# Kernel optimization log

Hardware: AMD Instinct MI355X
Metric: run time of the kernel (lower is better)

## Reference

```python
import jax, jax.numpy as jnp
import numpy as np
from jax import lax

# pywt 'db6' rec_lo (scaling filter). dec_lo = rec_lo[::-1]; pytorch_wavelets
# stores dec filters flipped for conv (=correlation), so analysis correlation
# filters are exactly rec_lo and rec_hi = qmf(rec_lo). Synthesis filters for
# conv_transpose are rec_lo/rec_hi unflipped -> same arrays.
_DB6 = np.array([0.11154074335008017, 0.4946238903983854, 0.7511339080215775,
                 0.3152503517092432, -0.22626469396516913, -0.12976686756709563,
                 0.09750160558707936, 0.02752286553001629, -0.031582039318031156,
                 0.0005538422009938016, 0.004777257511010651, -0.00107730108499558],
                dtype=np.float32)
_QMF = (_DB6[::-1].copy() * ((-1.0) ** np.arange(12))).astype(np.float32)
H0, H1 = jnp.asarray(_DB6), jnp.asarray(_QMF)
LF, J = 12, 3
BATCH, SEQ_LEN, CH = 128, 720, 321
COMP_L = [99, 365, 188, 99]   # [yl, yh1, yh2, yh3] for seq_len=720
OUT_L = [22, 57, 34, 22]      # same decomposition of red_len=104


def afb1d(x):
    """One-level analysis filter bank, mode='symmetric'. x: [B,C,N]."""
    B, C, N = x.shape
    out = (N + LF - 1) // 2                      # pywt dwt_coeff_len (symmetric)
    p = 2 * (out - 1) - N + LF
    xp = jnp.pad(x, ((0, 0), (0, 0), (p // 2, (p + 1) // 2)), mode='symmetric')
    w = jnp.stack([H0, H1])[:, None, :]          # [2,1,LF]
    y = lax.conv_general_dilated(xp.reshape(B * C, 1, -1), w, (2,), 'VALID',
                                 dimension_numbers=('NCH', 'OIH', 'NCH'))
    y = y.reshape(B, C, 2, out)
    return y[:, :, 0], y[:, :, 1]


def sfb1d(lo, hi):
    """One-level synthesis bank == conv_transpose1d(stride=2, padding=LF-2)."""
    B, C, Lin = lo.shape
    z = jnp.stack([lo, hi], axis=2).reshape(B * C, 2, Lin)
    w = jnp.stack([H0[::-1], H1[::-1]])[None]    # [1,2,LF], flipped for corr
    y = lax.conv_general_dilated(z, w, (1,), ((1, 1),), lhs_dilation=(2,),
                                 dimension_numbers=('NCH', 'OIH', 'NCH'))
    return y.reshape(B, C, -1)                   # length 2*Lin + 2 - LF


def sinusoidal_pe(n_pos, d):
    pos = jnp.arange(n_pos, dtype=jnp.float32)[:, None]
    div = jnp.exp(jnp.arange(0, d, 2, dtype=jnp.float32) * (-np.log(10000.0) / d))
    pe = jnp.zeros((n_pos, d), jnp.float32)
    pe = pe.at[:, 0::2].set(jnp.sin(pos * div))
    pe = pe.at[:, 1::2].set(jnp.cos(pos * div[: d // 2]))
    return pe


def _forward(x, qws, qbs, kws, kbs, pws, pbs, iws, als, bes):
    mean = lax.stop_gradient(jnp.mean(x, axis=1, keepdims=True))
    std = lax.stop_gradient(jnp.sqrt(jnp.var(x, axis=1, keepdims=True) + 1e-5))
    xc = jnp.transpose((x - mean) / std, (0, 2, 1))      # [B,C,L]
    yl, yh = xc, []
    for _ in range(J):
        yl, hi = afb1d(yl)
        yh.append(hi)
    decomps = [yl] + yh                                  # lengths COMP_L
    preds = []
    for i, comp in enumerate(decomps):
        B, C, L = comp.shape
        Q = jnp.tanh(comp @ qws[i].T + qbs[i])           # [B,C,L]
        K = jnp.tanh(comp @ kws[i].T + kbs[i])
        scores = jnp.einsum('bcl,bcs->bls', Q, K) / (L ** 0.5)
        weighted = jnp.mean(jnp.tanh(scores), axis=1)    # [B,S] (equal per channel)
        cum = jnp.flip(jnp.cumsum(jnp.flip(weighted, -1), -1), -1)
        P = jax.nn.softmax(cum * als[i][0], axis=-1)
        idxs = jnp.arange(L, dtype=jnp.float32)
        win = jnp.sum(P * idxs, axis=-1)[:, None, None]  # soft truncation [B,1,1]
        mask = jax.nn.sigmoid((idxs[None, None, :] - win) * bes[i][0])
        pred = (comp * mask) @ pws[i].T + pbs[i]         # [B,C,O]
        pred = jax.nn.softmax(iws[i], axis=1) * (pred + sinusoidal_pe(C, pred.shape[-1])[None])
        preds.append(pred)
    ll = preds[0]
    for h in preds[:0:-1]:                               # coarsest high band first
        if ll.shape[-1] > h.shape[-1]:
            ll = ll[..., : h.shape[-1]]
        ll = sfb1d(ll, h)
    return ll, mean, std


def setup_inputs() -> dict:
    key = jax.random.key(0)
    ks = jax.random.split(key, 64)
    inp = {'x': jax.random.normal(ks[0], (BATCH, SEQ_LEN, CH), jnp.float32)}
    k = 1
    for i, (L, O) in enumerate(zip(COMP_L, OUT_L)):
        s = 1.0 / np.sqrt(L)                             # torch Linear default init
        inp[f'qw{i}'] = jax.random.uniform(ks[k], (L, L), jnp.float32, -s, s); k += 1
        inp[f'qb{i}'] = jax.random.uniform(ks[k], (L,), jnp.float32, -s, s); k += 1
        inp[f'kw{i}'] = jax.random.uniform(ks[k], (L, L), jnp.float32, -s, s); k += 1
        inp[f'kb{i}'] = jax.random.uniform(ks[k], (L,), jnp.float32, -s, s); k += 1
        inp[f'pw{i}'] = jnp.full((O, L), 1.0 / L, jnp.float32)
        inp[f'pb{i}'] = jnp.zeros((O,), jnp.float32)
        inp[f'iw{i}'] = jnp.ones((1, CH, O), jnp.float32)
        inp[f'al{i}'] = jnp.full((1,), 10.0, jnp.float32)
        inp[f'be{i}'] = jnp.full((1,), 10.0, jnp.float32)
    return inp


def reference(x, qw0, qb0, kw0, kb0, pw0, pb0, iw0, al0, be0,
              qw1, qb1, kw1, kb1, pw1, pb1, iw1, al1, be1,
              qw2, qb2, kw2, kb2, pw2, pb2, iw2, al2, be2,
              qw3, qb3, kw3, kb3, pw3, pb3, iw3, al3, be3):
    return _forward(x, [qw0, qw1, qw2, qw3], [qb0, qb1, qb2, qb3],
                    [kw0, kw1, kw2, kw3], [kb0, kb1, kb2, kb3],
                    [pw0, pw1, pw2, pw3], [pb0, pb1, pb2, pb3],
                    [iw0, iw1, iw2, iw3], [al0, al1, al2, al3],
                    [be0, be1, be2, be3])
```

## Files before the change

kernel.cpp:

```cpp
#include <hip/hip_runtime.h>
#include <hip/hip_bf16.h>
#include <math.h>

namespace {
constexpr int kB  = 128;
constexpr int kC  = 321;
constexpr int kN0 = 720;
constexpr int kCp = 384;
}

typedef __attribute__((ext_vector_type(8))) short short8;
typedef __attribute__((ext_vector_type(4))) float floatx4;

__constant__ float c_h0[12] = {
  0.11154074335008017f, 0.4946238903983854f, 0.7511339080215775f,
  0.3152503517092432f, -0.22626469396516913f, -0.12976686756709563f,
  0.09750160558707936f, 0.02752286553001629f, -0.031582039318031156f,
  0.0005538422009938016f, 0.004777257511010651f, -0.00107730108499558f};
__constant__ float c_h1[12] = {
  -0.00107730108499558f, -0.004777257511010651f, 0.0005538422009938016f,
  0.031582039318031156f, 0.02752286553001629f, -0.09750160558707936f,
  -0.12976686756709563f, 0.22626469396516913f, 0.3152503517092432f,
  -0.7511339080215775f, 0.4946238903983854f, -0.11154074335008017f};
__constant__ float c_h0r[12] = {
  -0.00107730108499558f, 0.004777257511010651f, 0.0005538422009938016f,
  -0.031582039318031156f, 0.02752286553001629f, 0.09750160558707936f,
  -0.12976686756709563f, -0.22626469396516913f, 0.3152503517092432f,
  0.7511339080215775f, 0.4946238903983854f, 0.11154074335008017f};
__constant__ float c_h1r[12] = {
  -0.11154074335008017f, 0.4946238903983854f, -0.7511339080215775f,
  0.3152503517092432f, 0.22626469396516913f, -0.12976686756709563f,
  -0.09750160558707936f, 0.02752286553001629f, 0.031582039318031156f,
  0.0005538422009938016f, -0.004777257511010651f, -0.00107730108499558f};

__device__ __forceinline__ float fast_tanh(float x) {
  float e = __expf(2.f * x);
  return 1.f - 2.f / (e + 1.f);
}
__device__ __forceinline__ unsigned short f2b(float f) {
  __hip_bfloat16 h = __float2bfloat16(f);
  return __builtin_bit_cast(unsigned short, h);
}

__device__ __forceinline__ void gload16(const unsigned short* g, short* l) {
  __builtin_amdgcn_global_load_lds(
      (const __attribute__((address_space(1))) unsigned int*)g,
      (__attribute__((address_space(3))) unsigned int*)l, 16, 0, 0);
}

__global__ void __launch_bounds__(128) partial_ms_kernel(
    const float* __restrict__ x, float* __restrict__ ps, float* __restrict__ ps2) {
  int b = blockIdx.x, chunk = blockIdx.y;
  int c = blockIdx.z * 128 + threadIdx.x;
  if (c >= kC) return;
  const float* xb = x + (size_t)b * kN0 * kC + c;
  int t0 = chunk * 90;
  float s = 0.f, s2 = 0.f;
#pragma unroll 15
  for (int i = 0; i < 90; ++i) {
    float v = xb[(size_t)(t0 + i) * kC];
    s += v; s2 += v * v;
  }
  ps [(b * 8 + chunk) * kC + c] = s;
  ps2[(b * 8 + chunk) * kC + c] = s2;
}

__global__ void __launch_bounds__(256) finalize_ms_kernel(
    const float* __restrict__ ps, const float* __restrict__ ps2,
    float* __restrict__ mout, float* __restrict__ sout,
    float* __restrict__ meanw, float* __restrict__ invw) {
  int i = blockIdx.x * 256 + threadIdx.x;
  if (i >= kB * kC) return;
  int b = i / kC, c = i - b * kC;
  float s = 0.f, s2 = 0.f;
#pragma unroll
  for (int k = 0; k < 8; ++k) { s += ps[(b * 8 + k) * kC + c]; s2 += ps2[(b * 8 + k) * kC + c]; }
  float mean = s * (1.f / (float)kN0);
  float var = s2 * (1.f / (float)kN0) - mean * mean;
  float sd = sqrtf(var + 1e-5f);
  mout[i] = mean; sout[i] = sd;
  meanw[i] = mean; invw[i] = 1.f / sd;
}

__device__ __forceinline__ int sym_reflect(int t, int N) {
  t = (t < 0) ? (-1 - t) : t;
  t = (t >= N) ? (2 * N - 1 - t) : t;
  return t;
}

template <bool NORM, bool LO_F32, bool LO_BF16>
__global__ void __launch_bounds__(256) dwt_fused_kernel(
    const float* __restrict__ in, const float* __restrict__ meanw,
    const float* __restrict__ invw, float* __restrict__ loF,
    unsigned short* __restrict__ loB, unsigned short* __restrict__ hiB,
    int N, int L, int Lp) {
  __shared__ float xs[138][64];
  __shared__ unsigned short los[64][72];
  __shared__ unsigned short his[64][72];
  const int b = blockIdx.z;
  const int n0 = blockIdx.x * 64, c0 = blockIdx.y * 64;
  const int tid = threadIdx.x;
  const int cl = tid & 63, wv = tid >> 6;
  const int c = c0 + cl;
  const int t0 = 2 * n0 - 10;
  const float* ib = in + (size_t)b * N * kC;
  float mean = 0.f, inv = 1.f;
  if (NORM && c < kC) { mean = meanw[b * kC + c]; inv = invw[b * kC + c]; }
  for (int r = wv; r < 138; r += 4) {
    int t = sym_reflect(t0 + r, N);
    float v = (c < kC) ? ib[(size_t)t * kC + c] : 0.f;
    if (NORM) v = (v - mean) * inv;
    xs[r][cl] = v;
  }
  __syncthreads();
#pragma unroll 4
  for (int k = 0; k < 16; ++k) {
    int nl = wv + 4 * k;
    int n = n0 + nl;
    float a0 = 0.f, a1 = 0.f;
    int base = 2 * nl;
#pragma unroll
    for (int j = 0; j < 12; ++j) {
      float v = xs[base + j][cl];
      a0 += v * c_h0[j]; a1 += v * c_h1[j];
    }
    bool valid = (n < L) && (c < kC);
    if (LO_F32 && valid) loF[((size_t)b * L + n) * kC + c] = a0;
    if (LO_BF16) los[cl][nl] = f2b(valid ? a0 : 0.f);
    his[cl][nl] = f2b(valid ? a1 : 0.f);
  }
  __syncthreads();
  int row = tid >> 2, part = tid & 3;
  size_t dst = ((size_t)b * kCp + c0 + row) * Lp + n0 + part * 16;
  *(uint4*)(hiB + dst)     = *(const uint4*)&his[row][part * 16];
  *(uint4*)(hiB + dst + 8) = *(const uint4*)&his[row][part * 16 + 8];
  if (LO_BF16) {
    *(uint4*)(loB + dst)     = *(const uint4*)&los[row][part * 16];
    *(uint4*)(loB + dst + 8) = *(const uint4*)&los[row][part * 16 + 8];
  }
}

struct WcArgs { const float* src[8]; unsigned short* dst[8]; int L[8]; int Lp[8]; };
__global__ void __launch_bounds__(256) wconv_all_kernel(WcArgs a) {
  int lvl = blockIdx.y;
  int Lp = a.Lp[lvl], L = a.L[lvl];
  int i = blockIdx.x * 256 + threadIdx.x;
  if (i >= Lp * Lp) return;
  int p = i / Lp, l = i - p * Lp;
  a.dst[lvl][i] = f2b((p < L && l < L) ? a.src[lvl][(size_t)p * L + l] : 0.f);
}

template <int NT>
__device__ __forceinline__ void qk_kloop(
    short* smem, const unsigned short* s0, const unsigned short* s1,
    const unsigned short* s2, bool extra, int lo0, int lo1, int lo2,
    int ar, int bb, floatx4 (&acc)[2][4]) {
  gload16(s0, &smem[lo0]);
  gload16(s1, &smem[lo1]);
  if (extra) gload16(s2, &smem[lo2]);
  __syncthreads();
#pragma unroll
  for (int kt = 0; kt < NT; ++kt) {
    if (kt + 1 < NT) {
      const int phn = ((kt + 1) & 1) * 10240;
      const int go = (kt + 1) * 32;
      gload16(s0 + go, &smem[phn + lo0]);
      gload16(s1 + go, &smem[phn + lo1]);
      if (extra) gload16(s2 + go, &smem[phn + lo2]);
    }
    const int ph = (kt & 1) * 10240;
    short8 aq = *(const short8*)&smem[ph + ar];
    short8 ak = *(const short8*)&smem[ph + 4096 + ar];
    short8 bv[4];
#pragma unroll
    for (int ni = 0; ni < 4; ++ni)
      bv[ni] = *(const short8*)&smem[ph + 8192 + bb + ni * 512];
#pragma unroll
    for (int ni = 0; ni < 4; ++ni) {
      acc[0][ni] = __builtin_amdgcn_mfma_f32_16x16x32_bf16(aq, bv[ni], acc[0][ni], 0, 0, 0);
      acc[1][ni] = __builtin_amdgcn_mfma_f32_16x16x32_bf16(ak, bv[ni], acc[1][ni], 0, 0, 0);
    }
    __syncthreads();
  }
}

struct QKAllArgs {
  const unsigned short* W[8];
  const unsigned short* Xt[4];
  const float* bias[8];
  unsigned short* Y[8];
  int Lp[4], L[4], yOff[4];
};
__global__ void __launch_bounds__(512, 8) qk_all_kernel(QKAllArgs a) {
  const int y = blockIdx.y;
  const int lvl = (y >= a.yOff[1]) + (y >= a.yOff[2]) + (y >= a.yOff[3]);
  const int Lp = a.Lp[lvl], L = a.L[lvl];
  const int pBase = (y - a.yOff[lvl]) * 128;
  const unsigned short* W0 = a.W[2 * lvl]     + (size_t)pBase * Lp;
  const unsigned short* W1 = a.W[2 * lvl + 1] + (size_t)pBase * Lp;
  const int b = blockIdx.z;
  const int cBase = blockIdx.x * 64;
  const int tid = threadIdx.x;
  const int ln = tid & 63;
  const int w = __builtin_amdgcn_readfirstlane(tid >> 6);
  __shared__ short smem[2 * 320 * 32];
  floatx4 acc[2][4] = {};
  const unsigned short* Xb = a.Xt[lvl] + ((size_t)b * kCp + cBase) * Lp;
  const int lr = ln >> 2;
  const int kOfs = ((((ln & 3) - ((ln >> 3) & 3)) & 3)) * 8;
  const bool extra = (w < 4);
  const int o0 = 2 * w, o1 = 2 * w + 1;
  const unsigned short* s0 = (extra ? (W0 + (size_t)(o0 * 16 + lr) * Lp)
                                    : (W1 + (size_t)((o0 - 8) * 16 + lr) * Lp)) + kOfs;
  const unsigned short* s1 = (extra ? (W0 + (size_t)(o1 * 16 + lr) * Lp)
                                    : (W1 + (size_t)((o1 - 8) * 16 + lr) * Lp)) + kOfs;
  const unsigned short* s2 = Xb + (size_t)(w * 16 + lr) * Lp + kOfs;
  const int lo0 = o0 * 512, lo1 = o1 * 512, lo2 = (16 + w) * 512;
  const int sc = ((((ln >> 4) + ((ln >> 1) & 3)) & 3)) * 8;
  const int ar = (w * 16 + (ln & 15)) * 32 + sc;
  const int bb = (ln & 15) * 32 + sc;
  const int nt = (L + 31) >> 5;
  if (nt == 4)      qk_kloop<4>(smem, s0, s1, s2, extra, lo0, lo1, lo2, ar, bb, acc);
  else if (nt == 6) qk_kloop<6>(smem, s0, s1, s2, extra, lo0, lo1, lo2, ar, bb, acc);
  else              qk_kloop<12>(smem, s0, s1, s2, extra, lo0, lo1, lo2, ar, bb, acc);
  short* yq = smem;
  short* yk = smem + 8192;
#pragma unroll
  for (int s = 0; s < 2; ++s) {
    const float* bias = a.bias[2 * lvl + s];
    short* dstL = s ? yk : yq;
#pragma unroll
    for (int r = 0; r < 4; ++r) {
      int pl = w * 16 + (ln >> 4) * 4 + r;
      int p = pBase + pl;
      bool pv = (p < L);
      float bvf = pv ? bias[p] : 0.f;
#pragma unroll
      for (int ni = 0; ni < 4; ++ni) {
        int cl = ni * 16 + (ln & 15);
        float v = fast_tanh(acc[s][ni][r] + bvf);
        if (s == 1 && cBase + cl >= kC) v = 0.f;
        dstL[pl * 64 + (cl ^ ((pl & 7) << 3))] = (short)f2b(v);
      }
    }
  }
  __syncthreads();
#pragma unroll
  for (int s = 0; s < 2; ++s) {
    unsigned short* Yd = a.Y[2 * lvl + s];
    const short* srcL = s ? yk : yq;
#pragma unroll
    for (int j = 0; j < 2; ++j) {
      int idx = tid * 2 + j;
      int row = idx >> 3;
      if (pBase + row >= L) continue;
      int ch = idx & 7;
      int pch = ch ^ (row & 7);
      uint4 vv = *(const uint4*)&srcL[row * 64 + pch * 8];
      *(uint4*)(Yd + ((size_t)b * Lp + pBase + row) * kCp + cBase + ch * 8) = vv;
    }
  }
}

struct ScAllArgs {
  const unsigned short* Q[4]; const unsigned short* K[4];
  float* wgt[4];
  int Lp[4], L[4], tOff[4];
  float scale[4];
};
__global__ void __launch_bounds__(512, 8) scores_all_kernel(ScAllArgs a) {
  const int bid = blockIdx.x;
  const int wg = (bid & 7) * 240 + (bid >> 3);
  const int t = wg % 15;
  const int b = wg / 15;
  const int lvl = (t >= a.tOff[1]) + (t >= a.tOff[2]) + (t >= a.tOff[3]);
  const int rel = t - a.tOff[lvl];
  const int Lp = a.Lp[lvl], L = a.L[lvl];
  const int pt = Lp >> 7;
  const int sBase = (rel % pt) * 128;
  const int lBase = (rel / pt) * 128;
  const int tid = threadIdx.x;
  const int ln = tid & 63;
  const int w = __builtin_amdgcn_readfirstlane(tid >> 6);
  const int wm = w & 3, wn = w >> 2;
  __shared__ short smem[2 * 256 * 32];
  __shared__ float red[128];
  floatx4 acc[2][4] = {};
  const unsigned short* Qp = a.Q[lvl] + ((size_t)b * Lp + lBase) * kCp;
  const unsigned short* Kp = a.K[lvl] + ((size_t)b * Lp + sBase) * kCp;
  const int lr = ln >> 2;
  const int kOfs = ((((ln & 3) - ((ln >> 3) & 3)) & 3)) * 8;
  const int o0 = 2 * w, o1 = 2 * w + 1;
  const unsigned short* s0 = ((o0 < 8) ? (Qp + (size_t)(o0 * 16 + lr) * kCp)
                                       : (Kp + (size_t)((o0 - 8) * 16 + lr) * kCp)) + kOfs;
  const unsigned short* s1 = ((o1 < 8) ? (Qp + (size_t)(o1 * 16 + lr) * kCp)
                                       : (Kp + (size_t)((o1 - 8) * 16 + lr) * kCp)) + kOfs;
  const int lo0 = o0 * 512, lo1 = o1 * 512;
  const int sc = ((((ln >> 4) + ((ln >> 1) & 3)) & 3)) * 8;
  const int aBase = (wm * 32 + (ln & 15)) * 32 + sc;
  const int bBase = 4096 + (wn * 64 + (ln & 15)) * 32 + sc;
  gload16(s0, &smem[lo0]);
  gload16(s1, &smem[lo1]);
  if (tid < 128) red[tid] = 0.f;
  __syncthreads();
  constexpr int NT = (kC + 31) >> 5;
#pragma unroll
  for (int kt = 0; kt < NT; ++kt) {
    if (kt + 1 < NT) {
      const int phn = ((kt + 1) & 1) * 8192;
      const int go = (kt + 1) * 32;
      gload16(s0 + go, &smem[phn + lo0]);
      gload16(s1 + go, &smem[phn + lo1]);
    }
    const int ph = (kt & 1) * 8192;
    short8 av[2], bv[4];
#pragma unroll
    for (int mi = 0; mi < 2; ++mi)
      av[mi] = *(const short8*)&smem[ph + aBase + mi * 512];
#pragma unroll
    for (int ni = 0; ni < 4; ++ni)
      bv[ni] = *(const short8*)&smem[ph + bBase + ni * 512];
#pragma unroll
    for (int mi = 0; mi < 2; ++mi)
#pragma unroll
      for (int ni = 0; ni < 4; ++ni)
        acc[mi][ni] = __builtin_amdgcn_mfma_f32_16x16x32_bf16(av[mi], bv[ni], acc[mi][ni], 0, 0, 0);
    __syncthreads();
  }
  const float scale = a.scale[lvl];
#pragma unroll
  for (int ni = 0; ni < 4; ++ni) {
    float p = 0.f;
#pragma unroll
    for (int mi = 0; mi < 2; ++mi)
#pragma unroll
      for (int r = 0; r < 4; ++r) {
        int l = lBase + wm * 32 + mi * 16 + (ln >> 4) * 4 + r;
        if (l < L) p += fast_tanh(acc[mi][ni][r] * scale);
      }
    p += __shfl_xor(p, 16);
    p += __shfl_xor(p, 32);
    if ((ln & 48) == 0) atomicAdd(&red[wn * 64 + ni * 16 + (ln & 15)], p);
  }
  __syncthreads();
  if (tid < 128) {
    int s = sBase + tid;
    if (s < L) atomicAdd(&a.wgt[lvl][(size_t)b * L + s], red[tid]);
  }
}

struct WinIwArgs {
  const float* wgt[4]; const float* al[4]; const float* be[4];
  float* mask[4]; int L[4];
  const float* iw[4]; float* sm[4]; int O[4];
};
__global__ void __launch_bounds__(64) winiw_kernel(WinIwArgs a) {
  int bx = blockIdx.x;
  int lane = threadIdx.x;
  if (bx < 512) {
    int lvl = bx >> 7, b = bx & 127;
    int L = a.L[lvl];
    const float* wgt = a.wgt[lvl] + (size_t)b * L;
    float al = a.al[lvl][0], be = a.be[lvl][0];
    float invL = 1.f / (float)L;
    int chunk = (L + 63) >> 6;
    int s0 = lane * chunk;
    float v[6];
    float csum = 0.f;
    for (int i = chunk - 1; i >= 0; --i) {
      int s = s0 + i;
      float xv = (s < L) ? wgt[s] * invL : 0.f;
      csum += xv; v[i] = csum;
    }
    float tot = csum;
    for (int o = 1; o < 64; o <<= 1) {
      float t = __shfl_down(tot, o);
      if (lane + o < 64) tot += t;
    }
    float excl = tot - csum;
    float m = -1e30f;
    for (int i = 0; i < chunk; ++i)
      if (s0 + i < L) m = fmaxf(m, al * (v[i] + excl));
    for (int o = 32; o; o >>= 1) m = fmaxf(m, __shfl_xor(m, o));
    float sum = 0.f, num = 0.f;
    for (int i = 0; i < chunk; ++i) {
      int s = s0 + i;
      if (s < L) { float e = __expf(al * (v[i] + excl) - m); sum += e; num += e * (float)s; }
    }
    for (int o = 32; o; o >>= 1) { sum += __shfl_xor(sum, o); num += __shfl_xor(num, o); }
    float win = num / sum;
    float* mk = a.mask[lvl] + (size_t)b * L;
    for (int i = 0; i < chunk; ++i) {
      int s = s0 + i;
      if (s < L) mk[s] = 1.f / (1.f + __expf(-((float)s - win) * be));
    }
  } else {
    int x = bx - 512;
    int lvl, o;
    if (x < 22) { lvl = 0; o = x; }
    else if (x < 79) { lvl = 1; o = x - 22; }
    else if (x < 113) { lvl = 2; o = x - 79; }
    else { lvl = 3; o = x - 113; }
    int O = a.O[lvl];
    const float* iw = a.iw[lvl];
    float m = -1e30f;
    for (int c = lane; c < kC; c += 64) m = fmaxf(m, iw[c * O + o]);
    for (int k = 32; k; k >>= 1) m = fmaxf(m, __shfl_xor(m, k));
    float sum = 0.f;
    for (int c = lane; c < kC; c += 64) sum += __expf(iw[c * O + o] - m);
    for (int k = 32; k; k >>= 1) sum += __shfl_xor(sum, k);
    float inv = 1.f / sum;
    for (int c = lane; c < kC; c += 64) a.sm[lvl][c * O + o] = __expf(iw[c * O + o] - m) * inv;
  }
}

struct PredAllArgs {
  const unsigned short* Xt[4];
  const float* PW[4]; const float* PB[4]; const float* MK[4]; const float* SM[4];
  float* OUT[4];
  int L[4], Lp[4], O[4];
};
__global__ void __launch_bounds__(256) pred_all_kernel(PredAllArgs a) {
  const int lvl = blockIdx.y;
  const int L = a.L[lvl], Lp = a.Lp[lvl], O = a.O[lvl];
  const float* PW = a.PW[lvl];
  const int b = blockIdx.z;
  const int cBase = blockIdx.x * 128;
  const int tid = threadIdx.x;
  const int ln = tid & 63, w = tid >> 6;
  __shared__ short As[64 * 40];
  __shared__ short Bs[128 * 40];
  floatx4 acc[8] = {};
  const unsigned short* Xb = a.Xt[lvl] + ((size_t)b * kCp + cBase) * Lp;
  const float* mk = a.MK[lvl] + (size_t)b * L;
  for (int lc = 0; lc < Lp; lc += 32) {
    {
      int o = tid >> 2, j0 = (tid & 3) * 8;
      alignas(16) unsigned short tmp[8];
#pragma unroll
      for (int j = 0; j < 8; ++j) {
        int l = lc + j0 + j;
        float v = (o < O && l < L) ? PW[(size_t)o * L + l] * mk[l] : 0.f;
        tmp[j] = f2b(v);
      }
      *(uint4*)&As[o * 40 + j0] = *(const uint4*)tmp;
    }
#pragma unroll
    for (int q = 0; q < 2; ++q) {
      int ch = tid * 2 + q;
      int row = ch >> 2, pos = ch & 3;
      *(uint4*)(&Bs[row * 40 + pos * 8]) = *(const uint4*)(Xb + (size_t)row * Lp + lc + pos * 8);
    }
    __syncthreads();
    short8 av = *(const short8*)&As[(w * 16 + (ln & 15)) * 40 + (ln >> 4) * 8];
#pragma unroll
    for (int ni = 0; ni < 8; ++ni) {
      short8 bb = *(const short8*)&Bs[(ni * 16 + (ln & 15)) * 40 + (ln >> 4) * 8];
      acc[ni] = __builtin_amdgcn_mfma_f32_16x16x32_bf16(av, bb, acc[ni], 0, 0, 0);
    }
    __syncthreads();
  }
  const float negln = -logf(10000.f) / (float)O;
#pragma unroll
  for (int ni = 0; ni < 8; ++ni) {
    int c = cBase + ni * 16 + (ln & 15);
    if (c >= kC) continue;
#pragma unroll
    for (int r = 0; r < 4; ++r) {
      int o = w * 16 + (ln >> 4) * 4 + r;
      if (o >= O) continue;
      float dv = __expf(negln * (float)(2 * (o >> 1)));
      float ang = (float)c * dv;
      float pe = (o & 1) ? cosf(ang) : sinf(ang);
      a.OUT[lvl][((size_t)b * O + o) * kC + c] = a.SM[lvl][c * O + o] * (acc[ni][r] + a.PB[lvl][o] + pe);
    }
  }
}

__global__ void __launch_bounds__(256) sfb_fused_kernel(
    const float* __restrict__ P0, const float* __restrict__ P1,
    const float* __restrict__ P2, const float* __restrict__ P3,
    float* __restrict__ out) {
  __shared__ float p0s[22][32], p3s[22][32], p2s[34][32], p1s[57][32];
  __shared__ float r1s[34][32], r2s[58][32];
  __shared__ float outs[104][33];
  int b = blockIdx.y, c0 = blockIdx.x * 32;
  int tid = threadIdx.x;
  int cl = tid & 31, r = tid >> 5;
  int c = c0 + cl;
  bool cv = c < kC;
  for (int o = r; o < 22; o += 8) {
    p0s[o][cl] = cv ? P0[((size_t)b * 22 + o) * kC + c] : 0.f;
    p3s[o][cl] = cv ? P3[((size_t)b * 22 + o) * kC + c] : 0.f;
  }
  for (int o = r; o < 34; o += 8) p2s[o][cl] = cv ? P2[((size_t)b * 34 + o) * kC + c] : 0.f;
  for (int o = r; o < 57; o += 8) p1s[o][cl] = cv ? P1[((size_t)b * 57 + o) * kC + c] : 0.f;
  __syncthreads();
  for (int n = r; n < 34; n += 8) {
    float acc = 0.f;
#pragma unroll
    for (int j = 0; j < 12; ++j) {
      int m = n + j - 1;
      if (m < 0 || (m & 1)) continue;
      int i = m >> 1;
      if (i >= 22) continue;
      acc += c_h0r[j] * p0s[i][cl] + c_h1r[j] * p3s[i][cl];
    }
    r1s[n][cl] = acc;
  }
  __syncthreads();
  for (int n = r; n < 58; n += 8) {
    float acc = 0.f;
#pragma unroll
    for (int j = 0; j < 12; ++j) {
      int m = n + j - 1;
      if (m < 0 || (m & 1)) continue;
      int i = m >> 1;
      if (i >= 34) continue;
      acc += c_h0r[j] * r1s[i][cl] + c_h1r[j] * p2s[i][cl];
    }
    r2s[n][cl] = acc;
  }
  __syncthreads();
  for (int n = r; n < 104; n += 8) {
    float acc = 0.f;
#pragma unroll
    for (int j = 0; j < 12; ++j) {
      int m = n + j - 1;
      if (m < 0 || (m & 1)) continue;
      int i = m >> 1;
      if (i >= 57) continue;
      acc += c_h0r[j] * r2s[i][cl] + c_h1r[j] * p1s[i][cl];
    }
    outs[n][cl] = acc;
  }
  __syncthreads();
  for (int idx = tid; idx < 32 * 104; idx += 256) {
    int ci = idx / 104, n = idx - ci * 104;
    int cg = c0 + ci;
    if (cg < kC) out[((size_t)b * kC + cg) * 104 + n] = outs[n][ci];
  }
}

extern "C" void kernel_launch(void* const* d_in, const int* in_sizes, int n_in,
                              void* d_out, int out_size, void* d_ws, size_t ws_size,
                              hipStream_t stream) {
  (void)in_sizes; (void)n_in; (void)out_size; (void)ws_size;
  const float* x = (const float*)d_in[0];
  auto inp = [&](int lvl, int j) { return (const float*)d_in[1 + 9 * lvl + j]; };

  float* outf = (float*)d_out;
  float* mout = outf + (size_t)kB * kC * 104;
  float* sout = mout + (size_t)kB * kC;

  float* Wp = (float*)d_ws;
  size_t off = 0;
  auto alloc = [&](size_t n) { float* p = Wp + off; off += (n + 63) & ~(size_t)63; return p; };

  float* LO1 = alloc((size_t)kB * 365 * kC);
  float* LO2 = alloc((size_t)kB * 188 * kC);
  unsigned short* Xt1 = (unsigned short*)alloc((size_t)kB * kCp * 384 / 2);
  unsigned short* Xt2 = (unsigned short*)alloc((size_t)kB * kCp * 256 / 2);
  unsigned short* Xt0 = (unsigned short*)alloc((size_t)kB * kCp * 128 / 2);
  unsigned short* Xt3 = (unsigned short*)alloc((size_t)kB * kCp * 128 / 2);
  unsigned short* KbfAll = (unsigned short*)alloc((size_t)kB * kCp * 896 / 2);
  unsigned short* Wpv[8];
  for (int i = 0; i < 8; ++i)
    Wpv[i] = (unsigned short*)alloc((size_t)384 * 384 / 2);
  float* wgtAll = alloc((size_t)kB * (99 + 365 + 188 + 99));
  float* M0 = alloc((size_t)kB * 99);  float* M1 = alloc((size_t)kB * 365);
  float* M2 = alloc((size_t)kB * 188); float* M3 = alloc((size_t)kB * 99);
  float* S0 = alloc((size_t)kC * 22);  float* S1 = alloc((size_t)kC * 57);
  float* S2 = alloc((size_t)kC * 34);  float* S3 = alloc((size_t)kC * 22);
  float* P0 = alloc((size_t)kB * 22 * kC); float* P1 = alloc((size_t)kB * 57 * kC);
  float* P2 = alloc((size_t)kB * 34 * kC); float* P3 = alloc((size_t)kB * 22 * kC);
  float* ps   = alloc((size_t)kB * 8 * kC);
  float* ps2  = alloc((size_t)kB * 8 * kC);
  float* meanw = alloc((size_t)kB * kC);
  float* invw  = alloc((size_t)kB * kC);
  unsigned short* QbfAll = (unsigned short*)LO1;

  const int Lc[4]  = {99, 365, 188, 99};
  const int Lpv[4] = {128, 384, 256, 128};
  const int Ov[4]  = {22, 57, 34, 22};
  const int prefLp[4] = {0, 128, 512, 768};
  const int wOff[4] = {0, 99, 99 + 365, 99 + 365 + 188};
  unsigned short* Qlvl[4]; unsigned short* Klvl[4];
  for (int i = 0; i < 4; ++i) {
    Qlvl[i] = QbfAll + (size_t)kB * kCp * prefLp[i];
    Klvl[i] = KbfAll + (size_t)kB * kCp * prefLp[i];
  }
  const unsigned short* Xts[4] = {Xt0, Xt1, Xt2, Xt3};
  float* masks[4] = {M0, M1, M2, M3};
  float* smws[4]  = {S0, S1, S2, S3};
  float* preds[4] = {P0, P1, P2, P3};

  partial_ms_kernel<<<dim3(kB, 8, 3), 128, 0, stream>>>(x, ps, ps2);
  finalize_ms_kernel<<<(kB * kC + 255) / 256, 256, 0, stream>>>(ps, ps2, mout, sout, meanw, invw);

  dwt_fused_kernel<true, true, false><<<dim3(6, kCp / 64, kB), 256, 0, stream>>>(
      x, meanw, invw, LO1, nullptr, Xt1, kN0, 365, 384);
  dwt_fused_kernel<false, true, false><<<dim3(4, kCp / 64, kB), 256, 0, stream>>>(
      LO1, nullptr, nullptr, LO2, nullptr, Xt2, 365, 188, 256);
  dwt_fused_kernel<false, false, true><<<dim3(2, kCp / 64, kB), 256, 0, stream>>>(
      LO2, nullptr, nullptr, nullptr, Xt0, Xt3, 188, 99, 128);

  {
    WcArgs wa;
    for (int i = 0; i < 4; ++i) {
      wa.src[2 * i] = inp(i, 0); wa.src[2 * i + 1] = inp(i, 2);
      wa.dst[2 * i] = Wpv[2 * i]; wa.dst[2 * i + 1] = Wpv[2 * i + 1];
      wa.L[2 * i] = wa.L[2 * i + 1] = Lc[i];
      wa.Lp[2 * i] = wa.Lp[2 * i + 1] = Lpv[i];
    }
    wconv_all_kernel<<<dim3(576, 8), 256, 0, stream>>>(wa);
  }
  hipMemsetAsync(wgtAll, 0, (size_t)kB * (99 + 365 + 188 + 99) * sizeof(float), stream);

  {
    QKAllArgs qa;
    for (int i = 0; i < 4; ++i) {
      qa.W[2 * i] = Wpv[2 * i]; qa.W[2 * i + 1] = Wpv[2 * i + 1];
      qa.bias[2 * i] = inp(i, 1); qa.bias[2 * i + 1] = inp(i, 3);
      qa.Y[2 * i] = Qlvl[i]; qa.Y[2 * i + 1] = Klvl[i];
      qa.Xt[i] = Xts[i]; qa.Lp[i] = Lpv[i]; qa.L[i] = Lc[i];
    }
    qa.yOff[0] = 0; qa.yOff[1] = 1; qa.yOff[2] = 4; qa.yOff[3] = 6;
    qk_all_kernel<<<dim3(kCp / 64, 7, kB), 512, 0, stream>>>(qa);
  }

  {
    ScAllArgs sa;
    for (int i = 0; i < 4; ++i) {
      sa.Q[i] = Qlvl[i]; sa.K[i] = Klvl[i];
      sa.wgt[i] = wgtAll + (size_t)kB * wOff[i];
      sa.Lp[i] = Lpv[i]; sa.L[i] = Lc[i];
      sa.scale[i] = 1.0f / sqrtf((float)Lc[i]);
    }
    sa.tOff[0] = 0; sa.tOff[1] = 1; sa.tOff[2] = 10; sa.tOff[3] = 14;
    scores_all_kernel<<<15 * kB, 512, 0, stream>>>(sa);
  }

  {
    WinIwArgs wa;
    for (int i = 0; i < 4; ++i) {
      wa.wgt[i] = wgtAll + (size_t)kB * wOff[i];
      wa.al[i] = inp(i, 7); wa.be[i] = inp(i, 8);
      wa.mask[i] = masks[i]; wa.L[i] = Lc[i];
      wa.iw[i] = inp(i, 6); wa.sm[i] = smws[i]; wa.O[i] = Ov[i];
    }
    winiw_kernel<<<512 + 135, 64, 0, stream>>>(wa);
  }

  {
    PredAllArgs pa;
    for (int i = 0; i < 4; ++i) {
      pa.Xt[i] = Xts[i]; pa.PW[i] = inp(i, 4); pa.PB[i] = inp(i, 5);
      pa.MK[i] = masks[i]; pa.SM[i] = smws[i]; pa.OUT[i] = preds[i];
      pa.L[i] = Lc[i]; pa.Lp[i] = Lpv[i]; pa.O[i] = Ov[i];
    }
    pred_all_kernel<<<dim3(kCp / 128, 4, kB), 256, 0, stream>>>(pa);
  }

  sfb_fused_kernel<<<dim3(11, kB), 256, 0, stream>>>(P0, P1, P2, P3, outf);
}
```

Before: 751.1 us.

## Widen QK projection tile to 128 channels with 2x2 warp MFMA tiling

```diff
diff --git a/kernel.cpp b/kernel.cpp
--- a/kernel.cpp
+++ b/kernel.cpp
@@ -153,33 +153,38 @@
 template <int NT>
 __device__ __forceinline__ void qk_kloop(
     short* smem, const unsigned short* s0, const unsigned short* s1,
-    const unsigned short* s2, bool extra, int lo0, int lo1, int lo2,
-    int ar, int bb, floatx4 (&acc)[2][4]) {
+    const unsigned short* s2, int lo0, int lo1, int lo2,
+    int arB, int bbB, floatx4 (&acc)[2][2][4]) {
   gload16(s0, &smem[lo0]);
   gload16(s1, &smem[lo1]);
-  if (extra) gload16(s2, &smem[lo2]);
+  gload16(s2, &smem[lo2]);
   __syncthreads();
 #pragma unroll
   for (int kt = 0; kt < NT; ++kt) {
     if (kt + 1 < NT) {
-      const int phn = ((kt + 1) & 1) * 10240;
+      const int phn = ((kt + 1) & 1) * 12288;
       const int go = (kt + 1) * 32;
       gload16(s0 + go, &smem[phn + lo0]);
       gload16(s1 + go, &smem[phn + lo1]);
-      if (extra) gload16(s2 + go, &smem[phn + lo2]);
-    }
-    const int ph = (kt & 1) * 10240;
-    short8 aq = *(const short8*)&smem[ph + ar];
-    short8 ak = *(const short8*)&smem[ph + 4096 + ar];
-    short8 bv[4];
+      gload16(s2 + go, &smem[phn + lo2]);
+    }
+    const int ph = (kt & 1) * 12288;
+    short8 aq[2], ak[2], bv[4];
+#pragma unroll
+    for (int mi = 0; mi < 2; ++mi) {
+      aq[mi] = *(const short8*)&smem[ph + arB + mi * 512];
+      ak[mi] = *(const short8*)&smem[ph + 4096 + arB + mi * 512];
+    }
 #pragma unroll
     for (int ni = 0; ni < 4; ++ni)
-      bv[ni] = *(const short8*)&smem[ph + 8192 + bb + ni * 512];
-#pragma unroll
-    for (int ni = 0; ni < 4; ++ni) {
-      acc[0][ni] = __builtin_amdgcn_mfma_f32_16x16x32_bf16(aq, bv[ni], acc[0][ni], 0, 0, 0);
-      acc[1][ni] = __builtin_amdgcn_mfma_f32_16x16x32_bf16(ak, bv[ni], acc[1][ni], 0, 0, 0);
-    }
+      bv[ni] = *(const short8*)&smem[ph + 8192 + bbB + ni * 512];
+#pragma unroll
+    for (int mi = 0; mi < 2; ++mi)
+#pragma unroll
+      for (int ni = 0; ni < 4; ++ni) {
+        acc[0][mi][ni] = __builtin_amdgcn_mfma_f32_16x16x32_bf16(aq[mi], bv[ni], acc[0][mi][ni], 0, 0, 0);
+        acc[1][mi][ni] = __builtin_amdgcn_mfma_f32_16x16x32_bf16(ak[mi], bv[ni], acc[1][mi][ni], 0, 0, 0);
+      }
     __syncthreads();
   }
 }
@@ -191,7 +196,7 @@
   unsigned short* Y[8];
   int Lp[4], L[4], yOff[4];
 };
-__global__ void __launch_bounds__(512, 8) qk_all_kernel(QKAllArgs a) {
+__global__ void __launch_bounds__(512, 4) qk_all_kernel(QKAllArgs a) {
   const int y = blockIdx.y;
   const int lvl = (y >= a.yOff[1]) + (y >= a.yOff[2]) + (y >= a.yOff[3]);
   const int Lp = a.Lp[lvl], L = a.L[lvl];
@@ -199,66 +204,69 @@
   const unsigned short* W0 = a.W[2 * lvl]     + (size_t)pBase * Lp;
   const unsigned short* W1 = a.W[2 * lvl + 1] + (size_t)pBase * Lp;
   const int b = blockIdx.z;
-  const int cBase = blockIdx.x * 64;
+  const int cBase = blockIdx.x * 128;
   const int tid = threadIdx.x;
   const int ln = tid & 63;
   const int w = __builtin_amdgcn_readfirstlane(tid >> 6);
-  __shared__ short smem[2 * 320 * 32];
-  floatx4 acc[2][4] = {};
+  const int wm = w & 3, wn = w >> 2;
+  __shared__ short smem[2 * 384 * 32];
+  floatx4 acc[2][2][4] = {};
   const unsigned short* Xb = a.Xt[lvl] + ((size_t)b * kCp + cBase) * Lp;
   const int lr = ln >> 2;
   const int kOfs = ((((ln & 3) - ((ln >> 3) & 3)) & 3)) * 8;
-  const bool extra = (w < 4);
-  const int o0 = 2 * w, o1 = 2 * w + 1;
-  const unsigned short* s0 = (extra ? (W0 + (size_t)(o0 * 16 + lr) * Lp)
-                                    : (W1 + (size_t)((o0 - 8) * 16 + lr) * Lp)) + kOfs;
-  const unsigned short* s1 = (extra ? (W0 + (size_t)(o1 * 16 + lr) * Lp)
-                                    : (W1 + (size_t)((o1 - 8) * 16 + lr) * Lp)) + kOfs;
-  const unsigned short* s2 = Xb + (size_t)(w * 16 + lr) * Lp + kOfs;
-  const int lo0 = o0 * 512, lo1 = o1 * 512, lo2 = (16 + w) * 512;
+  const unsigned short* srcs[3];
+  int los[3];
+#pragma unroll
+  for (int i = 0; i < 3; ++i) {
+    int o = 3 * w + i;
+    const unsigned short* s = (o < 8)  ? (W0 + (size_t)(o * 16 + lr) * Lp)
+                            : (o < 16) ? (W1 + (size_t)((o - 8) * 16 + lr) * Lp)
+                                       : (Xb + (size_t)((o - 16) * 16 + lr) * Lp);
+    srcs[i] = s + kOfs;
+    los[i] = o * 512;
+  }
   const int sc = ((((ln >> 4) + ((ln >> 1) & 3)) & 3)) * 8;
-  const int ar = (w * 16 + (ln & 15)) * 32 + sc;
-  const int bb = (ln & 15) * 32 + sc;
+  const int arB = (wm * 32 + (ln & 15)) * 32 + sc;
+  const int bbB = (wn * 64 + (ln & 15)) * 32 + sc;
   const int nt = (L + 31) >> 5;
-  if (nt == 4)      qk_kloop<4>(smem, s0, s1, s2, extra, lo0, lo1, lo2, ar, bb, acc);
-  else if (nt == 6) qk_kloop<6>(smem, s0, s1, s2, extra, lo0, lo1, lo2, ar, bb, acc);
-  else              qk_kloop<12>(smem, s0, s1, s2, extra, lo0, lo1, lo2, ar, bb, acc);
-  short* yq = smem;
-  short* yk = smem + 8192;
+  if (nt == 4)      qk_kloop<4>(smem, srcs[0], srcs[1], srcs[2], los[0], los[1], los[2], arB, bbB, acc);
+  else if (nt == 6) qk_kloop<6>(smem, srcs[0], srcs[1], srcs[2], los[0], los[1], los[2], arB, bbB, acc);
+  else              qk_kloop<12>(smem, srcs[0], srcs[1], srcs[2], los[0], los[1], los[2], arB, bbB, acc);
+  short* bnc = smem;
 #pragma unroll
   for (int s = 0; s < 2; ++s) {
     const float* bias = a.bias[2 * lvl + s];
-    short* dstL = s ? yk : yq;
-#pragma unroll
-    for (int r = 0; r < 4; ++r) {
-      int pl = w * 16 + (ln >> 4) * 4 + r;
-      int p = pBase + pl;
-      bool pv = (p < L);
-      float bvf = pv ? bias[p] : 0.f;
-#pragma unroll
-      for (int ni = 0; ni < 4; ++ni) {
-        int cl = ni * 16 + (ln & 15);
-        float v = fast_tanh(acc[s][ni][r] + bvf);
-        if (s == 1 && cBase + cl >= kC) v = 0.f;
-        dstL[pl * 64 + (cl ^ ((pl & 7) << 3))] = (short)f2b(v);
+#pragma unroll
+    for (int mi = 0; mi < 2; ++mi) {
+#pragma unroll
+      for (int r = 0; r < 4; ++r) {
+        int pl = wm * 32 + mi * 16 + (ln >> 4) * 4 + r;
+        int p = pBase + pl;
+        bool pv = (p < L);
+        float bvf = pv ? bias[p] : 0.f;
+#pragma unroll
+        for (int ni = 0; ni < 4; ++ni) {
+          int cl = wn * 64 + ni * 16 + (ln & 15);
+          float v = fast_tanh(acc[s][mi][ni][r] + bvf);
+          if (s == 1 && cBase + cl >= kC) v = 0.f;
+          bnc[pl * 136 + (cl ^ ((pl & 7) << 3))] = (short)f2b(v);
+        }
       }
     }
-  }
-  __syncthreads();
-#pragma unroll
-  for (int s = 0; s < 2; ++s) {
+    __syncthreads();
     unsigned short* Yd = a.Y[2 * lvl + s];
-    const short* srcL = s ? yk : yq;
-#pragma unroll
-    for (int j = 0; j < 2; ++j) {
-      int idx = tid * 2 + j;
-      int row = idx >> 3;
-      if (pBase + row >= L) continue;
-      int ch = idx & 7;
-      int pch = ch ^ (row & 7);
-      uint4 vv = *(const uint4*)&srcL[row * 64 + pch * 8];
-      *(uint4*)(Yd + ((size_t)b * Lp + pBase + row) * kCp + cBase + ch * 8) = vv;
-    }
+#pragma unroll
+    for (int j = 0; j < 4; ++j) {
+      int idx = tid + j * 512;
+      int row = idx >> 4;
+      int ch = idx & 15;
+      if (pBase + row < L) {
+        int pch = ch ^ (row & 7);
+        uint4 vv = *(const uint4*)&bnc[row * 136 + pch * 8];
+        *(uint4*)(Yd + ((size_t)b * Lp + pBase + row) * kCp + cBase + ch * 8) = vv;
+      }
+    }
+    __syncthreads();
   }
 }
 
@@ -626,7 +634,7 @@
       qa.Xt[i] = Xts[i]; qa.Lp[i] = Lpv[i]; qa.L[i] = Lc[i];
     }
     qa.yOff[0] = 0; qa.yOff[1] = 1; qa.yOff[2] = 4; qa.yOff[3] = 6;
-    qk_all_kernel<<<dim3(kCp / 64, 7, kB), 512, 0, stream>>>(qa);
+    qk_all_kernel<<<dim3(kCp / 128, 7, kB), 512, 0, stream>>>(qa);
   }
 
   {
```

Result: no change. 759.2 us (+1.1%).
